# Optimization experiments

Hardware: AMD Instinct MI355X
Metric: run time of the kernel (lower is better)

The kernel has to match this reference:

```python
import jax, jax.numpy as jnp
import numpy as np

FACTOR = 5  # sampling factor from __init__


def setup_inputs() -> dict:
    key = jax.random.key(0)
    k1, k2, k3, k4 = jax.random.split(key, 4)
    B, L, H, D = 4, 2048, 8, 64
    S = min(FACTOR * int(np.ceil(np.log(L))), L)  # U_part = 40
    return {
        "queries": jax.random.normal(k1, (B, L, H, D), jnp.float32),
        "keys": jax.random.normal(k2, (B, L, H, D), jnp.float32),
        "values": jax.random.normal(k3, (B, L, H, D), jnp.float32),
        "index_sample": jax.random.randint(k4, (L, S), 0, L, jnp.int32),
    }


def reference(queries, keys, values, index_sample):
    B, L_Q, H, D = queries.shape
    L_K = keys.shape[1]
    Q = jnp.transpose(queries, (0, 2, 1, 3))  # [B,H,L_Q,D]
    K = jnp.transpose(keys, (0, 2, 1, 3))     # [B,H,L_K,D]
    V = jnp.transpose(values, (0, 2, 1, 3))   # [B,H,L_K,D]

    u = min(FACTOR * int(np.ceil(np.log(L_Q))), L_Q)  # n_top

    # --- _prob_QK: sampled QK to score queries, then top-u query selection ---
    # K_sample[b,h,q,s,:] = K[b,h,index_sample[q,s],:]  -> [B,H,L_Q,S,D]
    K_sample = K[:, :, index_sample, :]
    Q_K_sample = jnp.einsum('bhqd,bhqsd->bhqs', Q, K_sample)  # [B,H,L_Q,S]
    M = Q_K_sample.max(-1) - Q_K_sample.sum(-1) / L_K         # sparsity measure
    _, M_top = jax.lax.top_k(M, u)                            # [B,H,u] query indices

    Q_reduce = jnp.take_along_axis(Q, M_top[..., None], axis=2)  # [B,H,u,D]
    scale = 1.0 / np.sqrt(D)
    scores = jnp.einsum('bhud,bhkd->bhuk', Q_reduce, K) * scale  # [B,H,u,L_K]

    # --- _update_context causal mask: rows are the FIRST u rows of the full
    # triu(L_Q,L_Q) mask (faithful to original, which does NOT reindex by M_top)
    causal = jnp.triu(jnp.ones((u, L_Q), dtype=bool), 1)
    scores = jnp.where(causal[None, None], -jnp.inf, scores)
    attn = jax.nn.softmax(scores, axis=-1)
    upd = jnp.einsum('bhuk,bhkd->bhud', attn, V)  # [B,H,u,D]

    # --- _get_initial_context (mask_flag=True): running cumsum of V ---
    context = jnp.cumsum(V, axis=2)  # [B,H,L_Q,D]

    # scatter-overwrite selected query positions
    b = jnp.arange(B)[:, None, None]
    h = jnp.arange(H)[None, :, None]
    context = context.at[b, h, M_top].set(upd)

    return jnp.transpose(context, (0, 2, 1, 3))  # [B,L_Q,H,D]
```

## Files before the change

### kernel.cpp

```cpp
#include <hip/hip_runtime.h>
#include <stdint.h>

constexpr int B = 4, L = 2048, H = 8, D = 64, S = 40, U = 40;
constexpr int HD = H * D;
constexpr int NC = 64;
constexpr int CL = L / NC;
constexpr int NBLK = 256;

__device__ __forceinline__ unsigned mono(float v) {
    unsigned u = __float_as_uint(v);
    return (u & 0x80000000u) ? ~u : (u | 0x80000000u);
}

__device__ __forceinline__ void grid_barrier(int* cnt, int idx) {
    __syncthreads();
    if (threadIdx.x == 0) {
        __threadfence();
        atomicAdd(&cnt[idx * 32], 1);
        while (__hip_atomic_load(&cnt[idx * 32], __ATOMIC_RELAXED,
                                 __HIP_MEMORY_SCOPE_AGENT) < NBLK)
            __builtin_amdgcn_s_sleep(2);
        __threadfence();
    }
    __syncthreads();
}

__global__ __launch_bounds__(512) void k_fused(
    const float4* __restrict__ Q4, const float4* __restrict__ K4,
    const float* __restrict__ V, const int* __restrict__ idxs,
    float* __restrict__ Mg, int* __restrict__ flags, float* __restrict__ upd,
    float* __restrict__ partial, int* __restrict__ cnt, float* __restrict__ out)
{
    __shared__ float4 Ms4[512];
    __shared__ unsigned long long cnd[8 * U];
    __shared__ int top_idx[U];
    __shared__ __align__(16) float Qs[U * 68];
    __shared__ __align__(16) float Ks[U * 68];
    __shared__ __align__(16) float Vs[U * 68];
    __shared__ float P[U * 41];

    int bid = blockIdx.x;
    int tid = threadIdx.x;
    int b   = (bid & 7) >> 1;
    int sub = ((bid >> 3) << 1) | (bid & 1);
    int c   = sub;

    {
        int w = tid >> 6, lane = tid & 63;
        int dd = lane & 7;
        for (int j = 0; j < 4; ++j) {
            int q = sub * 32 + w * 4 + j;
            const float4* qrow = Q4 + (size_t)(b * L + q) * 128;
            float4 qa = qrow[2 * lane], qb = qrow[2 * lane + 1];
            int v_idx = idxs[q * S + (lane < S ? lane : 0)];
            float mx = -INFINITY, sm = 0.f;
            #pragma unroll 8
            for (int s = 0; s < S; ++s) {
                int ki = __shfl(v_idx, s);
                const float4* krow = K4 + (size_t)(b * L + ki) * 128;
                float4 ka = krow[2 * lane], kb = krow[2 * lane + 1];
                float dt = qa.x * ka.x + qa.y * ka.y + qa.z * ka.z + qa.w * ka.w
                         + qb.x * kb.x + qb.y * kb.y + qb.z * kb.z + qb.w * kb.w;
                dt += __shfl_xor(dt, 1);
                dt += __shfl_xor(dt, 2);
                dt += __shfl_xor(dt, 4);
                mx = fmaxf(mx, dt);
                sm += dt;
            }
            if (dd == 0) {
                int h = lane >> 3;
                Mg[(size_t)(b * 8 + h) * L + q] = mx - sm * (1.0f / (float)L);
            }
        }
    }
    {
        const float* vp = V + ((size_t)(b * L + c * CL)) * HD + tid;
        float s = 0.f;
        #pragma unroll
        for (int l = 0; l < CL; ++l) s += vp[(size_t)l * HD];
        partial[((size_t)b * NC + c) * HD + tid] = s;
    }
    if (tid < 256) {
        int h = tid >> 5, l0 = c * CL + (tid & 31);
        flags[(size_t)(b * 8 + h) * L + l0] = 0;
    }

    grid_barrier(cnt, 0);

    if (sub < 8) {
        int h = sub, bh = b * 8 + h;
        Ms4[tid] = ((const float4*)(Mg + (size_t)bh * L))[tid];
        __syncthreads();

        {
            int w = tid >> 6, lane = tid & 63;
            float4 v = Ms4[w * 64 + lane];
            unsigned m[4] = { mono(v.x), mono(v.y), mono(v.z), mono(v.w) };
            int rank[4] = { 0, 0, 0, 0 };
            #pragma unroll 4
            for (int src = 0; src < 64; ++src) {
                #pragma unroll
                for (int slot = 0; slot < 4; ++slot) {
                    unsigned bm = __shfl(m[slot], src);
                    int bj = src * 4 + slot;
                    #pragma unroll
                    for (int s2 = 0; s2 < 4; ++s2) {
                        int myj = lane * 4 + s2;
                        rank[s2] += (bm > m[s2]) || (bm == m[s2] && bj < myj);
                    }
                }
            }
            int j0 = w * 256 + lane * 4;
            #pragma unroll
            for (int s2 = 0; s2 < 4; ++s2)
                if (rank[s2] < U)
                    cnd[w * U + rank[s2]] = ((unsigned long long)m[s2] << 32)
                                          | (unsigned)(~(unsigned)(j0 + s2));
        }
        __syncthreads();

        if (tid < 8 * U) {
            unsigned long long ka = cnd[tid];
            int ra = 0;
            for (int j = 0; j < 8 * U; ++j) ra += (cnd[j] > ka);
            if (ra < U) {
                int qi = (int)(~(unsigned)ka);
                top_idx[ra] = qi;
                flags[(size_t)bh * L + qi] = ra + 1;
            }
        }
        __syncthreads();

        const float4* V4 = (const float4*)V;
        for (int i2 = tid; i2 < U * 16; i2 += 512) {
            int r = i2 >> 4, d4 = i2 & 15;
            size_t kvb = (size_t)(b * L + r) * 128 + h * 16 + d4;
            *(float4*)(Ks + r * 68 + d4 * 4) = K4[kvb];
            *(float4*)(Vs + r * 68 + d4 * 4) = V4[kvb];
            *(float4*)(Qs + r * 68 + d4 * 4) =
                Q4[(size_t)(b * L + top_idx[r]) * 128 + h * 16 + d4];
        }
        __syncthreads();

        const float scale = 0.125f;
        for (int p = tid; p < U * U; p += 512) {
            int r = p / U, k = p - r * U;
            if (k <= r) {
                float acc = 0.f;
                #pragma unroll
                for (int d = 0; d < D; d += 4) {
                    float4 a = *(const float4*)(Qs + r * 68 + d);
                    float4 cc = *(const float4*)(Ks + k * 68 + d);
                    acc += a.x * cc.x + a.y * cc.y + a.z * cc.z + a.w * cc.w;
                }
                P[r * 41 + k] = acc * scale;
            }
        }
        __syncthreads();

        if (tid < U) {
            int r = tid;
            float mval = -INFINITY;
            for (int k = 0; k <= r; ++k) mval = fmaxf(mval, P[r * 41 + k]);
            float ssum = 0.f;
            for (int k = 0; k <= r; ++k) {
                float e = expf(P[r * 41 + k] - mval);
                P[r * 41 + k] = e;
                ssum += e;
            }
            float inv = 1.f / ssum;
            for (int k = 0; k <= r; ++k) P[r * 41 + k] *= inv;
        }
        __syncthreads();

        for (int t = tid; t < U * D; t += 512) {
            int r = t >> 6, d = t & 63;
            float acc = 0.f;
            for (int k = 0; k <= r; ++k) acc += P[r * 41 + k] * Vs[k * 68 + d];
            upd[((size_t)bh * U + r) * D + d] = acc;
        }
    }

    float acc = 0.f;
    for (int cc = 0; cc < c; ++cc)
        acc += partial[((size_t)b * NC + cc) * HD + tid];

    grid_barrier(cnt, 1);

    {
        int h = tid >> 6, d = tid & 63;
        const float* vp = V + ((size_t)(b * L + c * CL)) * HD + tid;
        float*       op = out + ((size_t)(b * L + c * CL)) * HD + tid;
        const int*   fp = flags + (size_t)(b * 8 + h) * L + c * CL;
        const float* up = upd + (size_t)(b * 8 + h) * U * D + d;
        #pragma unroll 4
        for (int l = 0; l < CL; ++l) {
            acc += vp[(size_t)l * HD];
            int f = fp[l];
            op[(size_t)l * HD] = f ? up[(size_t)(f - 1) * D] : acc;
        }
    }
}

extern "C" void kernel_launch(void* const* d_in, const int* in_sizes, int n_in,
                              void* d_out, int out_size, void* d_ws, size_t ws_size,
                              hipStream_t stream)
{
    const float* Q   = (const float*)d_in[0];
    const float* K   = (const float*)d_in[1];
    const float* V   = (const float*)d_in[2];
    const int*  idxs = (const int*)d_in[3];
    float* out = (float*)d_out;

    char* ws = (char*)d_ws;
    float* Mg      = (float*)(ws);
    int*   flags   = (int*)  (ws + 262144);
    float* upd     = (float*)(ws + 524288);
    float* partial = (float*)(ws + 851968);
    int*   cnt     = (int*)  (ws + 1376256);

    hipMemsetAsync(cnt, 0, 256, stream);
    k_fused<<<NBLK, 512, 0, stream>>>((const float4*)Q, (const float4*)K, V, idxs,
                                      Mg, flags, upd, partial, cnt, out);
}
```

Baseline: 202.9 us.

## Double block size to 1024 threads and split work across halves

Grows each block from 512 to 1024 threads. Each wavefront now scores two queries at once, interleaving their independent gathered K loads for more memory-level parallelism. The V prefix-sum chunks are split into two 16-row halves with a finer partials array, so the cumsum scan and the output pass use twice the threads. The cost is more per-block registers under launch_bounds(1024,4), a longer serial partial-sum prefix loop per thread, and grid-barrier spinning with larger blocks.

```diff
diff --git a/kernel.cpp b/kernel.cpp
--- a/kernel.cpp
+++ b/kernel.cpp
@@ -25,11 +25,16 @@
     __syncthreads();
 }
 
-__global__ __launch_bounds__(512) void k_fused(
+__device__ __forceinline__ float dot8(float4 a, float4 b, float4 c, float4 d) {
+    return a.x * c.x + a.y * c.y + a.z * c.z + a.w * c.w
+         + b.x * d.x + b.y * d.y + b.z * d.z + b.w * d.w;
+}
+
+__global__ __launch_bounds__(1024, 4) void k_fused(
     const float4* __restrict__ Q4, const float4* __restrict__ K4,
     const float* __restrict__ V, const int* __restrict__ idxs,
     float* __restrict__ Mg, int* __restrict__ flags, float* __restrict__ upd,
-    float* __restrict__ partial, int* __restrict__ cnt, float* __restrict__ out)
+    float* __restrict__ partial2, int* __restrict__ cnt, float* __restrict__ out)
 {
     __shared__ float4 Ms4[512];
     __shared__ unsigned long long cnd[8 * U];
@@ -48,37 +53,47 @@
     {
         int w = tid >> 6, lane = tid & 63;
         int dd = lane & 7;
-        for (int j = 0; j < 4; ++j) {
-            int q = sub * 32 + w * 4 + j;
-            const float4* qrow = Q4 + (size_t)(b * L + q) * 128;
-            float4 qa = qrow[2 * lane], qb = qrow[2 * lane + 1];
-            int v_idx = idxs[q * S + (lane < S ? lane : 0)];
-            float mx = -INFINITY, sm = 0.f;
-            #pragma unroll 8
-            for (int s = 0; s < S; ++s) {
-                int ki = __shfl(v_idx, s);
-                const float4* krow = K4 + (size_t)(b * L + ki) * 128;
-                float4 ka = krow[2 * lane], kb = krow[2 * lane + 1];
-                float dt = qa.x * ka.x + qa.y * ka.y + qa.z * ka.z + qa.w * ka.w
-                         + qb.x * kb.x + qb.y * kb.y + qb.z * kb.z + qb.w * kb.w;
-                dt += __shfl_xor(dt, 1);
-                dt += __shfl_xor(dt, 2);
-                dt += __shfl_xor(dt, 4);
-                mx = fmaxf(mx, dt);
-                sm += dt;
-            }
-            if (dd == 0) {
-                int h = lane >> 3;
-                Mg[(size_t)(b * 8 + h) * L + q] = mx - sm * (1.0f / (float)L);
-            }
-        }
-    }
-    {
-        const float* vp = V + ((size_t)(b * L + c * CL)) * HD + tid;
+        int q0 = sub * 32 + w * 2;
+        const float4* qrow0 = Q4 + (size_t)(b * L + q0) * 128;
+        const float4* qrow1 = qrow0 + 128;
+        float4 qa0 = qrow0[2 * lane], qb0 = qrow0[2 * lane + 1];
+        float4 qa1 = qrow1[2 * lane], qb1 = qrow1[2 * lane + 1];
+        int li = (lane < S ? lane : 0);
+        int vi0 = idxs[q0 * S + li];
+        int vi1 = idxs[(q0 + 1) * S + li];
+        const float4* kbase = K4 + (size_t)b * L * 128;
+        float mx0 = -INFINITY, sm0 = 0.f, mx1 = -INFINITY, sm1 = 0.f;
+        #pragma unroll 4
+        for (int s = 0; s < S; ++s) {
+            const float4* kr0 = kbase + (size_t)__shfl(vi0, s) * 128;
+            const float4* kr1 = kbase + (size_t)__shfl(vi1, s) * 128;
+            float4 ka0 = kr0[2 * lane], kb0 = kr0[2 * lane + 1];
+            float4 ka1 = kr1[2 * lane], kb1 = kr1[2 * lane + 1];
+            float d0 = dot8(qa0, qb0, ka0, kb0);
+            float d1 = dot8(qa1, qb1, ka1, kb1);
+            d0 += __shfl_xor(d0, 1);
+            d1 += __shfl_xor(d1, 1);
+            d0 += __shfl_xor(d0, 2);
+            d1 += __shfl_xor(d1, 2);
+            d0 += __shfl_xor(d0, 4);
+            d1 += __shfl_xor(d1, 4);
+            mx0 = fmaxf(mx0, d0);  sm0 += d0;
+            mx1 = fmaxf(mx1, d1);  sm1 += d1;
+        }
+        if (dd == 0) {
+            int h = lane >> 3;
+            float* mrow = Mg + (size_t)(b * 8 + h) * L + q0;
+            mrow[0] = mx0 - sm0 * (1.0f / (float)L);
+            mrow[1] = mx1 - sm1 * (1.0f / (float)L);
+        }
+    }
+    {
+        int half = tid >> 9, col = tid & 511;
+        const float* vp = V + ((size_t)(b * L + c * CL + half * 16)) * HD + col;
         float s = 0.f;
         #pragma unroll
-        for (int l = 0; l < CL; ++l) s += vp[(size_t)l * HD];
-        partial[((size_t)b * NC + c) * HD + tid] = s;
+        for (int l = 0; l < 16; ++l) s += vp[(size_t)l * HD];
+        partial2[(((size_t)b * NC + c) * 2 + half) * HD + col] = s;
     }
     if (tid < 256) {
         int h = tid >> 5, l0 = c * CL + (tid & 31);
@@ -89,10 +104,10 @@
 
     if (sub < 8) {
         int h = sub, bh = b * 8 + h;
-        Ms4[tid] = ((const float4*)(Mg + (size_t)bh * L))[tid];
-        __syncthreads();
-
-        {
+        if (tid < 512) Ms4[tid] = ((const float4*)(Mg + (size_t)bh * L))[tid];
+        __syncthreads();
+
+        if (tid < 512) {
             int w = tid >> 6, lane = tid & 63;
             float4 v = Ms4[w * 64 + lane];
             unsigned m[4] = { mono(v.x), mono(v.y), mono(v.z), mono(v.w) };
@@ -132,8 +147,8 @@
         __syncthreads();
 
         const float4* V4 = (const float4*)V;
-        for (int i2 = tid; i2 < U * 16; i2 += 512) {
-            int r = i2 >> 4, d4 = i2 & 15;
+        if (tid < U * 16) {
+            int r = tid >> 4, d4 = tid & 15;
             size_t kvb = (size_t)(b * L + r) * 128 + h * 16 + d4;
             *(float4*)(Ks + r * 68 + d4 * 4) = K4[kvb];
             *(float4*)(Vs + r * 68 + d4 * 4) = V4[kvb];
@@ -143,7 +158,7 @@
         __syncthreads();
 
         const float scale = 0.125f;
-        for (int p = tid; p < U * U; p += 512) {
+        for (int p = tid; p < U * U; p += 1024) {
             int r = p / U, k = p - r * U;
             if (k <= r) {
                 float acc = 0.f;
@@ -173,7 +188,7 @@
         }
         __syncthreads();
 
-        for (int t = tid; t < U * D; t += 512) {
+        for (int t = tid; t < U * D; t += 1024) {
             int r = t >> 6, d = t & 63;
             float acc = 0.f;
             for (int k = 0; k <= r; ++k) acc += P[r * 41 + k] * Vs[k * 68 + d];
@@ -182,19 +197,27 @@
     }
 
     float acc = 0.f;
-    for (int cc = 0; cc < c; ++cc)
-        acc += partial[((size_t)b * NC + cc) * HD + tid];
+    {
+        int half = tid >> 9, col = tid & 511;
+        int key = c * 2 + half;
+        const float* pp = partial2 + (size_t)b * NC * 2 * HD + col;
+        #pragma unroll 4
+        for (int j = 0; j < key; ++j)
+            acc += pp[(size_t)j * HD];
+    }
 
     grid_barrier(cnt, 1);
 
     {
-        int h = tid >> 6, d = tid & 63;
-        const float* vp = V + ((size_t)(b * L + c * CL)) * HD + tid;
-        float*       op = out + ((size_t)(b * L + c * CL)) * HD + tid;
-        const int*   fp = flags + (size_t)(b * 8 + h) * L + c * CL;
+        int half = tid >> 9, col = tid & 511;
+        int h = col >> 6, d = col & 63;
+        int r0 = c * CL + half * 16;
+        const float* vp = V + ((size_t)(b * L + r0)) * HD + col;
+        float*       op = out + ((size_t)(b * L + r0)) * HD + col;
+        const int*   fp = flags + (size_t)(b * 8 + h) * L + r0;
         const float* up = upd + (size_t)(b * 8 + h) * U * D + d;
         #pragma unroll 4
-        for (int l = 0; l < CL; ++l) {
+        for (int l = 0; l < 16; ++l) {
             acc += vp[(size_t)l * HD];
             int f = fp[l];
             op[(size_t)l * HD] = f ? up[(size_t)(f - 1) * D] : acc;
@@ -213,13 +236,13 @@
     float* out = (float*)d_out;
 
     char* ws = (char*)d_ws;
-    float* Mg      = (float*)(ws);
-    int*   flags   = (int*)  (ws + 262144);
-    float* upd     = (float*)(ws + 524288);
-    float* partial = (float*)(ws + 851968);
-    int*   cnt     = (int*)  (ws + 1376256);
+    float* Mg       = (float*)(ws);
+    int*   flags    = (int*)  (ws + 262144);
+    float* upd      = (float*)(ws + 524288);
+    float* partial2 = (float*)(ws + 851968);
+    int*   cnt      = (int*)  (ws + 1900544);
 
     hipMemsetAsync(cnt, 0, 256, stream);
-    k_fused<<<NBLK, 512, 0, stream>>>((const float4*)Q, (const float4*)K, V, idxs,
-                                      Mg, flags, upd, partial, cnt, out);
-}
+    k_fused<<<NBLK, 1024, 0, stream>>>((const float4*)Q, (const float4*)K, V, idxs,
+                                       Mg, flags, upd, partial2, cnt, out);
+}
```

Result: faster. 192.8 us (-4.9%).

## Quadruple grid to 1024 blocks with one query per wave and 4-way K gather unroll

Applied to the files above, without the earlier changes.

Raises the persistent grid from 256 to 1024 blocks (NC=256 chunks of 8 rows), so each wave scores one query and gathers four sampled K rows per iteration for more memory-level parallelism. Shared-memory staging of M and V is removed to cut LDS use for higher occupancy (launch bounds 512,8), and the prefix over chunk partials is 4-way unrolled. The risk is that all 1024 blocks must be co-resident for the spin grid barrier, and the serial partial prefix grows to up to 255 loads per thread.

```diff
diff --git a/kernel.cpp b/kernel.cpp
--- a/kernel.cpp
+++ b/kernel.cpp
@@ -3,9 +3,9 @@
 
 constexpr int B = 4, L = 2048, H = 8, D = 64, S = 40, U = 40;
 constexpr int HD = H * D;
-constexpr int NC = 64;
+constexpr int NC = 256;
 constexpr int CL = L / NC;
-constexpr int NBLK = 256;
+constexpr int NBLK = 1024;
 
 __device__ __forceinline__ unsigned mono(float v) {
     unsigned u = __float_as_uint(v);
@@ -19,24 +19,27 @@
         atomicAdd(&cnt[idx * 32], 1);
         while (__hip_atomic_load(&cnt[idx * 32], __ATOMIC_RELAXED,
                                  __HIP_MEMORY_SCOPE_AGENT) < NBLK)
-            __builtin_amdgcn_s_sleep(2);
+            __builtin_amdgcn_s_sleep(8);
         __threadfence();
     }
     __syncthreads();
 }
 
-__global__ __launch_bounds__(512) void k_fused(
+__device__ __forceinline__ float dot8(float4 a, float4 b, float4 c, float4 d) {
+    return a.x * c.x + a.y * c.y + a.z * c.z + a.w * c.w
+         + b.x * d.x + b.y * d.y + b.z * d.z + b.w * d.w;
+}
+
+__global__ __launch_bounds__(512, 8) void k_fused(
     const float4* __restrict__ Q4, const float4* __restrict__ K4,
     const float* __restrict__ V, const int* __restrict__ idxs,
     float* __restrict__ Mg, int* __restrict__ flags, float* __restrict__ upd,
     float* __restrict__ partial, int* __restrict__ cnt, float* __restrict__ out)
 {
-    __shared__ float4 Ms4[512];
     __shared__ unsigned long long cnd[8 * U];
     __shared__ int top_idx[U];
     __shared__ __align__(16) float Qs[U * 68];
     __shared__ __align__(16) float Ks[U * 68];
-    __shared__ __align__(16) float Vs[U * 68];
     __shared__ float P[U * 41];
 
     int bid = blockIdx.x;
@@ -48,29 +51,37 @@
     {
         int w = tid >> 6, lane = tid & 63;
         int dd = lane & 7;
-        for (int j = 0; j < 4; ++j) {
-            int q = sub * 32 + w * 4 + j;
-            const float4* qrow = Q4 + (size_t)(b * L + q) * 128;
-            float4 qa = qrow[2 * lane], qb = qrow[2 * lane + 1];
-            int v_idx = idxs[q * S + (lane < S ? lane : 0)];
-            float mx = -INFINITY, sm = 0.f;
-            #pragma unroll 8
-            for (int s = 0; s < S; ++s) {
-                int ki = __shfl(v_idx, s);
-                const float4* krow = K4 + (size_t)(b * L + ki) * 128;
-                float4 ka = krow[2 * lane], kb = krow[2 * lane + 1];
-                float dt = qa.x * ka.x + qa.y * ka.y + qa.z * ka.z + qa.w * ka.w
-                         + qb.x * kb.x + qb.y * kb.y + qb.z * kb.z + qb.w * kb.w;
-                dt += __shfl_xor(dt, 1);
-                dt += __shfl_xor(dt, 2);
-                dt += __shfl_xor(dt, 4);
-                mx = fmaxf(mx, dt);
-                sm += dt;
-            }
-            if (dd == 0) {
-                int h = lane >> 3;
-                Mg[(size_t)(b * 8 + h) * L + q] = mx - sm * (1.0f / (float)L);
-            }
+        int q = sub * 8 + w;
+        const float4* qrow = Q4 + (size_t)(b * L + q) * 128;
+        float4 qa = qrow[2 * lane], qb = qrow[2 * lane + 1];
+        int vi = idxs[q * S + (lane < S ? lane : 0)];
+        const float4* kbase = K4 + (size_t)b * L * 128;
+        float mx = -INFINITY, sm = 0.f;
+        for (int it = 0; it < S; it += 4) {
+            const float4* r0 = kbase + (size_t)__shfl(vi, it + 0) * 128;
+            const float4* r1 = kbase + (size_t)__shfl(vi, it + 1) * 128;
+            const float4* r2 = kbase + (size_t)__shfl(vi, it + 2) * 128;
+            const float4* r3 = kbase + (size_t)__shfl(vi, it + 3) * 128;
+            float4 a0 = r0[2 * lane], e0 = r0[2 * lane + 1];
+            float4 a1 = r1[2 * lane], e1 = r1[2 * lane + 1];
+            float4 a2 = r2[2 * lane], e2 = r2[2 * lane + 1];
+            float4 a3 = r3[2 * lane], e3 = r3[2 * lane + 1];
+            float d0 = dot8(qa, qb, a0, e0);
+            float d1 = dot8(qa, qb, a1, e1);
+            float d2 = dot8(qa, qb, a2, e2);
+            float d3 = dot8(qa, qb, a3, e3);
+            d0 += __shfl_xor(d0, 1);  d1 += __shfl_xor(d1, 1);
+            d2 += __shfl_xor(d2, 1);  d3 += __shfl_xor(d3, 1);
+            d0 += __shfl_xor(d0, 2);  d1 += __shfl_xor(d1, 2);
+            d2 += __shfl_xor(d2, 2);  d3 += __shfl_xor(d3, 2);
+            d0 += __shfl_xor(d0, 4);  d1 += __shfl_xor(d1, 4);
+            d2 += __shfl_xor(d2, 4);  d3 += __shfl_xor(d3, 4);
+            mx = fmaxf(fmaxf(fmaxf(fmaxf(mx, d0), d1), d2), d3);
+            sm += (d0 + d1) + (d2 + d3);
+        }
+        if (dd == 0) {
+            int h = lane >> 3;
+            Mg[(size_t)(b * 8 + h) * L + q] = mx - sm * (1.0f / (float)L);
         }
     }
     {
@@ -80,8 +91,8 @@
         for (int l = 0; l < CL; ++l) s += vp[(size_t)l * HD];
         partial[((size_t)b * NC + c) * HD + tid] = s;
     }
-    if (tid < 256) {
-        int h = tid >> 5, l0 = c * CL + (tid & 31);
+    if (tid < 64) {
+        int h = tid >> 3, l0 = c * CL + (tid & 7);
         flags[(size_t)(b * 8 + h) * L + l0] = 0;
     }
 
@@ -89,12 +100,10 @@
 
     if (sub < 8) {
         int h = sub, bh = b * 8 + h;
-        Ms4[tid] = ((const float4*)(Mg + (size_t)bh * L))[tid];
-        __syncthreads();
 
         {
             int w = tid >> 6, lane = tid & 63;
-            float4 v = Ms4[w * 64 + lane];
+            float4 v = ((const float4*)(Mg + (size_t)bh * L))[w * 64 + lane];
             unsigned m[4] = { mono(v.x), mono(v.y), mono(v.z), mono(v.w) };
             int rank[4] = { 0, 0, 0, 0 };
             #pragma unroll 4
@@ -131,12 +140,10 @@
         }
         __syncthreads();
 
-        const float4* V4 = (const float4*)V;
         for (int i2 = tid; i2 < U * 16; i2 += 512) {
             int r = i2 >> 4, d4 = i2 & 15;
-            size_t kvb = (size_t)(b * L + r) * 128 + h * 16 + d4;
-            *(float4*)(Ks + r * 68 + d4 * 4) = K4[kvb];
-            *(float4*)(Vs + r * 68 + d4 * 4) = V4[kvb];
+            *(float4*)(Ks + r * 68 + d4 * 4) =
+                K4[(size_t)(b * L + r) * 128 + h * 16 + d4];
             *(float4*)(Qs + r * 68 + d4 * 4) =
                 Q4[(size_t)(b * L + top_idx[r]) * 128 + h * 16 + d4];
         }
@@ -175,25 +182,39 @@
 
         for (int t = tid; t < U * D; t += 512) {
             int r = t >> 6, d = t & 63;
+            const float* vrow = V + ((size_t)(b * L) * 8 + h) * 64 + d;
             float acc = 0.f;
-            for (int k = 0; k <= r; ++k) acc += P[r * 41 + k] * Vs[k * 68 + d];
+            for (int k = 0; k <= r; ++k)
+                acc += P[r * 41 + k] * vrow[(size_t)k * HD];
             upd[((size_t)bh * U + r) * D + d] = acc;
         }
     }
 
-    float acc = 0.f;
-    for (int cc = 0; cc < c; ++cc)
-        acc += partial[((size_t)b * NC + cc) * HD + tid];
+    float acc;
+    {
+        const float* pp = partial + (size_t)b * NC * HD + tid;
+        float a0 = 0.f, a1 = 0.f, a2 = 0.f, a3 = 0.f;
+        int j = 0;
+        for (; j + 4 <= c; j += 4) {
+            a0 += pp[(size_t)(j + 0) * HD];
+            a1 += pp[(size_t)(j + 1) * HD];
+            a2 += pp[(size_t)(j + 2) * HD];
+            a3 += pp[(size_t)(j + 3) * HD];
+        }
+        for (; j < c; ++j) a0 += pp[(size_t)j * HD];
+        acc = (a0 + a1) + (a2 + a3);
+    }
 
     grid_barrier(cnt, 1);
 
     {
         int h = tid >> 6, d = tid & 63;
-        const float* vp = V + ((size_t)(b * L + c * CL)) * HD + tid;
-        float*       op = out + ((size_t)(b * L + c * CL)) * HD + tid;
-        const int*   fp = flags + (size_t)(b * 8 + h) * L + c * CL;
+        int r0 = c * CL;
+        const float* vp = V + ((size_t)(b * L + r0)) * HD + tid;
+        float*       op = out + ((size_t)(b * L + r0)) * HD + tid;
+        const int*   fp = flags + (size_t)(b * 8 + h) * L + r0;
         const float* up = upd + (size_t)(b * 8 + h) * U * D + d;
-        #pragma unroll 4
+        #pragma unroll
         for (int l = 0; l < CL; ++l) {
             acc += vp[(size_t)l * HD];
             int f = fp[l];
@@ -217,7 +238,7 @@
     int*   flags   = (int*)  (ws + 262144);
     float* upd     = (float*)(ws + 524288);
     float* partial = (float*)(ws + 851968);
-    int*   cnt     = (int*)  (ws + 1376256);
+    int*   cnt     = (int*)  (ws + 2949120);
 
     hipMemsetAsync(cnt, 0, 256, stream);
     k_fused<<<NBLK, 512, 0, stream>>>((const float4*)Q, (const float4*)K, V, idxs,
```

New measurement: 449.9 us. 122% more time.
